# Optimization experiments

Measured on AMD Instinct MI355X. Metric: run time of the kernel, lower is better.

Reference implementation:

```python
import jax, jax.numpy as jnp
import numpy as np

N_NODES = 50000
N_EDGES = 800000
IN_CH = 128
OUT_CH = 32
HID = 2 * OUT_CH  # 64


def setup_inputs() -> dict:
    key = jax.random.key(0)
    ks = jax.random.split(key, 8)
    x = jax.random.normal(ks[0], (N_NODES, IN_CH), dtype=jnp.float32)
    edge_index = jax.random.randint(ks[1], (2, N_EDGES), 0, N_NODES, dtype=jnp.int32)
    s1 = 1.0 / np.sqrt(IN_CH)
    s2 = 1.0 / np.sqrt(HID)
    W1 = jax.random.normal(ks[2], (IN_CH, HID), dtype=jnp.float32) * s1
    b1 = jnp.zeros((HID,), dtype=jnp.float32)
    W_mu = jax.random.normal(ks[3], (HID, OUT_CH), dtype=jnp.float32) * s2
    b_mu = jnp.zeros((OUT_CH,), dtype=jnp.float32)
    W_logstd = jax.random.normal(ks[4], (HID, OUT_CH), dtype=jnp.float32) * s2
    b_logstd = jnp.zeros((OUT_CH,), dtype=jnp.float32)
    return {"x": x, "edge_index": edge_index, "W1": W1, "b1": b1,
            "W_mu": W_mu, "b_mu": b_mu, "W_logstd": W_logstd, "b_logstd": b_logstd}


def _gcn_norm(edge_index, n, dtype):
    # PyG GCNConv: add self-loops, symmetric normalization D^-1/2 A D^-1/2
    loops = jnp.arange(n, dtype=edge_index.dtype)
    src = jnp.concatenate([edge_index[0], loops])
    dst = jnp.concatenate([edge_index[1], loops])
    deg = jax.ops.segment_sum(jnp.ones_like(dst, dtype=dtype), dst, num_segments=n)
    deg_inv_sqrt = jnp.where(deg > 0, jax.lax.rsqrt(deg), 0.0)
    norm = deg_inv_sqrt[src] * deg_inv_sqrt[dst]  # [E+N]
    return src, dst, norm


def _gcn_conv(x, W, b, src, dst, norm, n):
    h = x @ W                        # transform first (in >= out)
    msg = h[src] * norm[:, None]     # gather + scale, [E+N, out]
    out = jax.ops.segment_sum(msg, dst, num_segments=n)
    return out + b


def reference(x, edge_index, W1, b1, W_mu, b_mu, W_logstd, b_logstd):
    n = x.shape[0]
    src, dst, norm = _gcn_norm(edge_index, n, x.dtype)
    h = jax.nn.relu(_gcn_conv(x, W1, b1, src, dst, norm, n))
    mu = _gcn_conv(h, W_mu, b_mu, src, dst, norm, n)
    logstd = _gcn_conv(h, W_logstd, b_logstd, src, dst, norm, n)
    return mu, logstd
```

## Files before the change

kernel.cpp:

```cpp
#include <hip/hip_runtime.h>
#include <hip/hip_fp16.h>

#define N_NODES 50000
#define N_EDGES 800000
#define IN_CH 128
#define HID 64
#define OUT_CH 32
#define CAP 64
#define ZROW N_NODES
#define PART_SZ 6250

union H4 { uint2 u; __half2 h[2]; };

__global__ __launch_bounds__(256) void k_scatter(const int* __restrict__ ei,
                                                 int* cur, unsigned short* __restrict__ pk,
                                                 unsigned* zA, unsigned* zB) {
    if (blockIdx.x == 0) {
        int t = threadIdx.x;
        if (t < 32) zA[t] = 0u;
        else if (t < 64) zB[t - 32] = 0u;
    }
    int part = blockIdx.x & 7;
    int g = (blockIdx.x >> 3) * 256 + threadIdx.x;
    if (g >= N_EDGES / 2) return;
    int2 dd = ((const int2*)(ei + N_EDGES))[g];
    bool a0 = (unsigned)(dd.x - part * PART_SZ) < (unsigned)PART_SZ;
    bool a1 = (unsigned)(dd.y - part * PART_SZ) < (unsigned)PART_SZ;
    if (!a0 && !a1) return;
    int2 ss = ((const int2*)ei)[g];
    if (a0) {
        int n = atomicAdd(&cur[dd.x], 1);
        int slot = (n < 32) ? (((n & 3) << 3) | (n >> 2)) : n;
        pk[(dd.x << 6) + slot] = (unsigned short)ss.x;
    }
    if (a1) {
        int n = atomicAdd(&cur[dd.y], 1);
        int slot = (n < 32) ? (((n & 3) << 3) | (n >> 2)) : n;
        pk[(dd.y << 6) + slot] = (unsigned short)ss.y;
    }
}

__global__ __launch_bounds__(256) void k_mm1(const float* __restrict__ x,
                                             const float* __restrict__ W1,
                                             const int* __restrict__ cur,
                                             __half* __restrict__ t1) {
    __shared__ float4 ws[64 * 16];
    __shared__ float  xsT[64 * 64];
    int t = threadIdx.x;
    int n0 = blockIdx.x * 64;
    int lane = t & 63, wv_ = t >> 6;
    int ni = lane >> 2;
    int cq = ((lane & 3) << 2) + wv_;
    const float4* W4 = (const float4*)W1;
    const float4* x4 = (const float4*)x;
    float4 acc0 = {0,0,0,0}, acc1 = acc0, acc2 = acc0, acc3 = acc0;
#pragma unroll
    for (int kt = 0; kt < 2; ++kt) {
        __syncthreads();
#pragma unroll
        for (int i = 0; i < 4; ++i) {
            int L = i * 256 + t;
            ws[L] = W4[kt * 1024 + L];
            int n = L >> 4, q = L & 15;
            int ng = n0 + n; if (ng >= N_NODES) ng = N_NODES - 1;
            float4 v = x4[ng * 32 + kt * 16 + q];
            int fb = q * 256 + (((n >> 2) ^ q) << 2) + (n & 3);
            xsT[fb]       = v.x;
            xsT[fb + 64]  = v.y;
            xsT[fb + 128] = v.z;
            xsT[fb + 192] = v.w;
        }
        __syncthreads();
        const float4* xsT4 = (const float4*)xsT;
#pragma unroll 8
        for (int k = 0; k < 64; ++k) {
            float4 xv = xsT4[k * 16 + (ni ^ (k >> 2))];
            float4 wvv = ws[k * 16 + cq];
            acc0.x += xv.x * wvv.x; acc0.y += xv.x * wvv.y; acc0.z += xv.x * wvv.z; acc0.w += xv.x * wvv.w;
            acc1.x += xv.y * wvv.x; acc1.y += xv.y * wvv.y; acc1.z += xv.y * wvv.z; acc1.w += xv.y * wvv.w;
            acc2.x += xv.z * wvv.x; acc2.y += xv.z * wvv.y; acc2.z += xv.z * wvv.z; acc2.w += xv.z * wvv.w;
            acc3.x += xv.w * wvv.x; acc3.y += xv.w * wvv.y; acc3.z += xv.w * wvv.z; acc3.w += xv.w * wvv.w;
        }
    }
    int nb = n0 + 4 * ni;
    if (nb < N_NODES) {
        int4 c4 = *(const int4*)(cur + nb);
        float d0 = rsqrtf((float)c4.x + 1.0f);
        float d1 = rsqrtf((float)c4.y + 1.0f);
        float d2 = rsqrtf((float)c4.z + 1.0f);
        float d3 = rsqrtf((float)c4.w + 1.0f);
        uint2* o2 = (uint2*)t1;
        H4 v;
        v.h[0] = __floats2half2_rn(d0 * acc0.x, d0 * acc0.y);
        v.h[1] = __floats2half2_rn(d0 * acc0.z, d0 * acc0.w);
        o2[(nb + 0) * 16 + cq] = v.u;
        v.h[0] = __floats2half2_rn(d1 * acc1.x, d1 * acc1.y);
        v.h[1] = __floats2half2_rn(d1 * acc1.z, d1 * acc1.w);
        o2[(nb + 1) * 16 + cq] = v.u;
        v.h[0] = __floats2half2_rn(d2 * acc2.x, d2 * acc2.y);
        v.h[1] = __floats2half2_rn(d2 * acc2.z, d2 * acc2.w);
        o2[(nb + 2) * 16 + cq] = v.u;
        v.h[0] = __floats2half2_rn(d3 * acc3.x, d3 * acc3.y);
        v.h[1] = __floats2half2_rn(d3 * acc3.z, d3 * acc3.w);
        o2[(nb + 3) * 16 + cq] = v.u;
    }
}

__global__ __launch_bounds__(256) void k_agg(const unsigned short* __restrict__ pk,
                                             const int* __restrict__ cur,
                                             const __half* __restrict__ in,
                                             const float* __restrict__ bias,
                                             __half* __restrict__ out,
                                             int apply_relu) {
    int wave = (blockIdx.x * 256 + threadIdx.x) >> 6;
    if (wave >= N_NODES / 2) return;
    int lane = threadIdx.x & 63;
    int half = lane >> 5;
    int eg = (lane >> 3) & 3;
    int cs = lane & 7;
    int w = wave * 2 + half;
    int cnt = cur[w];
    int rowb = w << 6;
    const uint4* __restrict__ inv = (const uint4*)in;

    uint4 pp = *(const uint4*)(pk + rowb + (eg << 3));
    const unsigned short* us = (const unsigned short*)&pp;
    int sidx[8];
#pragma unroll
    for (int j = 0; j < 8; ++j)
        sidx[j] = (eg + 4 * j < cnt) ? (int)us[j] : ZROW;
    int sself = (eg == 0) ? w : ZROW;
    uint4 r0 = inv[sidx[0] * 8 + cs];
    uint4 r1 = inv[sidx[1] * 8 + cs];
    uint4 r2 = inv[sidx[2] * 8 + cs];
    uint4 r3 = inv[sidx[3] * 8 + cs];
    uint4 r4 = inv[sidx[4] * 8 + cs];
    uint4 r5 = inv[sidx[5] * 8 + cs];
    uint4 r6 = inv[sidx[6] * 8 + cs];
    uint4 r7 = inv[sidx[7] * 8 + cs];
    uint4 rs = inv[sself * 8 + cs];
    float acc[8] = {0,0,0,0,0,0,0,0};
#define ACC8(R) { const __half2* h2 = (const __half2*)&(R); float2 f;          \
        f = __half22float2(h2[0]); acc[0] += f.x; acc[1] += f.y;               \
        f = __half22float2(h2[1]); acc[2] += f.x; acc[3] += f.y;               \
        f = __half22float2(h2[2]); acc[4] += f.x; acc[5] += f.y;               \
        f = __half22float2(h2[3]); acc[6] += f.x; acc[7] += f.y; }
    ACC8(r0); ACC8(r1); ACC8(r2); ACC8(r3);
    ACC8(r4); ACC8(r5); ACC8(r6); ACC8(r7);
    ACC8(rs);

    for (int n = 32 + eg; n < cnt; n += 4) {
        int s = (int)pk[rowb + n];
        uint4 r = inv[s * 8 + cs];
        ACC8(r);
    }
#undef ACC8
#pragma unroll
    for (int m = 8; m <= 16; m <<= 1)
#pragma unroll
        for (int i = 0; i < 8; ++i) acc[i] += __shfl_xor(acc[i], m, 64);
    if (eg == 0) {
        float dw = rsqrtf((float)cnt + 1.0f);
        if (apply_relu) {
            float4 b0 = ((const float4*)bias)[2 * cs];
            float4 b1v = ((const float4*)bias)[2 * cs + 1];
            acc[0] = dw * fmaxf(dw * acc[0] + b0.x, 0.f);
            acc[1] = dw * fmaxf(dw * acc[1] + b0.y, 0.f);
            acc[2] = dw * fmaxf(dw * acc[2] + b0.z, 0.f);
            acc[3] = dw * fmaxf(dw * acc[3] + b0.w, 0.f);
            acc[4] = dw * fmaxf(dw * acc[4] + b1v.x, 0.f);
            acc[5] = dw * fmaxf(dw * acc[5] + b1v.y, 0.f);
            acc[6] = dw * fmaxf(dw * acc[6] + b1v.z, 0.f);
            acc[7] = dw * fmaxf(dw * acc[7] + b1v.w, 0.f);
        } else {
#pragma unroll
            for (int i = 0; i < 8; ++i) acc[i] *= dw;
        }
        __half2 o[4];
        o[0] = __floats2half2_rn(acc[0], acc[1]);
        o[1] = __floats2half2_rn(acc[2], acc[3]);
        o[2] = __floats2half2_rn(acc[4], acc[5]);
        o[3] = __floats2half2_rn(acc[6], acc[7]);
        ((uint4*)out)[w * 8 + cs] = *(const uint4*)o;
    }
}

__global__ __launch_bounds__(256) void k_mm2(const __half* __restrict__ agg2,
                                             const float* __restrict__ Wmu,
                                             const float* __restrict__ bmu,
                                             const float* __restrict__ Wls,
                                             const float* __restrict__ bls,
                                             float* __restrict__ out) {
    __shared__ float4 ws[64 * 16];
    __shared__ float  xsT[64 * 64];
    int t = threadIdx.x;
    int n0 = blockIdx.x * 64;
    int lane = t & 63, wv_ = t >> 6;
    int ni = lane >> 2;
    int cq = ((lane & 3) << 2) + wv_;
    const float4* Wm4 = (const float4*)Wmu;
    const float4* Wl4 = (const float4*)Wls;
    const uint2*  x2  = (const uint2*)agg2;
#pragma unroll
    for (int i = 0; i < 4; ++i) {
        int L = i * 256 + t;
        int k = L >> 4, c = L & 15;
        ws[L] = (c < 8) ? Wm4[k * 8 + c] : Wl4[k * 8 + (c - 8)];
        int n = L >> 4, q = L & 15;
        int ng = n0 + n; if (ng >= N_NODES) ng = N_NODES - 1;
        H4 hv; hv.u = x2[ng * 16 + q];
        float2 f0 = __half22float2(hv.h[0]), f1 = __half22float2(hv.h[1]);
        int fb = q * 256 + (((n >> 2) ^ q) << 2) + (n & 3);
        xsT[fb]       = f0.x;
        xsT[fb + 64]  = f0.y;
        xsT[fb + 128] = f1.x;
        xsT[fb + 192] = f1.y;
    }
    float4 b = (cq < 8) ? ((const float4*)bmu)[cq] : ((const float4*)bls)[cq - 8];
    float4 acc0 = b, acc1 = b, acc2 = b, acc3 = b;
    __syncthreads();
    const float4* xsT4 = (const float4*)xsT;
#pragma unroll 8
    for (int k = 0; k < 64; ++k) {
        float4 xv = xsT4[k * 16 + (ni ^ (k >> 2))];
        float4 wvv = ws[k * 16 + cq];
        acc0.x += xv.x * wvv.x; acc0.y += xv.x * wvv.y; acc0.z += xv.x * wvv.z; acc0.w += xv.x * wvv.w;
        acc1.x += xv.y * wvv.x; acc1.y += xv.y * wvv.y; acc1.z += xv.y * wvv.z; acc1.w += xv.y * wvv.w;
        acc2.x += xv.z * wvv.x; acc2.y += xv.z * wvv.y; acc2.z += xv.z * wvv.z; acc2.w += xv.z * wvv.w;
        acc3.x += xv.w * wvv.x; acc3.y += xv.w * wvv.y; acc3.z += xv.w * wvv.z; acc3.w += xv.w * wvv.w;
    }
    int nb = n0 + 4 * ni;
    if (nb < N_NODES) {
        float4* o4 = (float4*)out;
        long base_off = (cq < 8) ? 0 : (long)N_NODES * 8;
        int cq8 = cq & 7;
        o4[base_off + (long)(nb + 0) * 8 + cq8] = acc0;
        o4[base_off + (long)(nb + 1) * 8 + cq8] = acc1;
        o4[base_off + (long)(nb + 2) * 8 + cq8] = acc2;
        o4[base_off + (long)(nb + 3) * 8 + cq8] = acc3;
    }
}

extern "C" void kernel_launch(void* const* d_in, const int* in_sizes, int n_in,
                              void* d_out, int out_size, void* d_ws, size_t ws_size,
                              hipStream_t stream) {
    const float* x   = (const float*)d_in[0];
    const int*   ei  = (const int*)  d_in[1];
    const float* W1  = (const float*)d_in[2];
    const float* b1  = (const float*)d_in[3];
    const float* Wmu = (const float*)d_in[4];
    const float* bmu = (const float*)d_in[5];
    const float* Wls = (const float*)d_in[6];
    const float* bls = (const float*)d_in[7];
    float* out = (float*)d_out;

    int*   cur  = (int*)d_ws;
    unsigned short* pk = (unsigned short*)((int*)d_ws + 50176);
    __half* bufA = (__half*)((int*)d_ws + 1650176);
    __half* bufB = (__half*)((int*)d_ws + 3250304);
    __half* bufC = (__half*)((int*)d_ws + 4850432);

    hipMemsetAsync(d_ws, 0, 200000, stream);
    k_scatter <<<1563 * 8, 256, 0, stream>>>(ei, cur, pk,
                   (unsigned*)(bufA + (size_t)ZROW * HID),
                   (unsigned*)(bufB + (size_t)ZROW * HID));
    k_mm1 <<<782, 256, 0, stream>>>(x, W1, cur, bufA);
    k_agg <<<6250, 256, 0, stream>>>(pk, cur, bufA, b1, bufB, 1);
    k_agg <<<6250, 256, 0, stream>>>(pk, cur, bufB, nullptr, bufC, 0);
    k_mm2 <<<782, 256, 0, stream>>>(bufC, Wmu, bmu, Wls, bls, out);
}
```

Baseline: 184.4 us.

## Replace 8-pass partitioned edge scatter with two-pass bucket-then-scatter CSR build

Edge insertion into per-destination adjacency lists used to run 8 partitioned passes, each rereading the whole edge list and keeping only destinations in its node range. Now one kernel reads every edge once and bins packed (dst,src) records into per-block segment buffers by destination partition, using shared-memory counters. A second kernel is ordered by bucket so that its atomics and pk writes stay local to one partition range. This removes 7 of the 8 rereads of edge_index at the cost of an extra kernel launch and a round trip of the packed records through memory.

Result: no change. 187.6 us (+1.8%).

```diff
diff --git a/kernel.cpp b/kernel.cpp
--- a/kernel.cpp
+++ b/kernel.cpp
@@ -9,35 +9,65 @@
 #define CAP 64
 #define ZROW N_NODES
 #define PART_SZ 6250
+#define NSEG 1563
+#define SEGCAP 128
 
 union H4 { uint2 u; __half2 h[2]; };
 
-__global__ __launch_bounds__(256) void k_scatter(const int* __restrict__ ei,
-                                                 int* cur, unsigned short* __restrict__ pk,
-                                                 unsigned* zA, unsigned* zB) {
+__global__ __launch_bounds__(256) void k_bucket(const int* __restrict__ ei,
+                                                int* cur, int* __restrict__ segcnt,
+                                                unsigned* __restrict__ segbuf,
+                                                unsigned short* __restrict__ pk,
+                                                unsigned* zA, unsigned* zB) {
+    __shared__ int lcnt[8];
+    int t = threadIdx.x;
     if (blockIdx.x == 0) {
-        int t = threadIdx.x;
         if (t < 32) zA[t] = 0u;
         else if (t < 64) zB[t - 32] = 0u;
     }
-    int part = blockIdx.x & 7;
-    int g = (blockIdx.x >> 3) * 256 + threadIdx.x;
-    if (g >= N_EDGES / 2) return;
-    int2 dd = ((const int2*)(ei + N_EDGES))[g];
-    bool a0 = (unsigned)(dd.x - part * PART_SZ) < (unsigned)PART_SZ;
-    bool a1 = (unsigned)(dd.y - part * PART_SZ) < (unsigned)PART_SZ;
-    if (!a0 && !a1) return;
-    int2 ss = ((const int2*)ei)[g];
-    if (a0) {
-        int n = atomicAdd(&cur[dd.x], 1);
-        int slot = (n < 32) ? (((n & 3) << 3) | (n >> 2)) : n;
-        pk[(dd.x << 6) + slot] = (unsigned short)ss.x;
-    }
-    if (a1) {
-        int n = atomicAdd(&cur[dd.y], 1);
-        int slot = (n < 32) ? (((n & 3) << 3) | (n >> 2)) : n;
-        pk[(dd.y << 6) + slot] = (unsigned short)ss.y;
-    }
+    if (t < 8) lcnt[t] = 0;
+    __syncthreads();
+    int g = blockIdx.x * 256 + t;
+    if (g < N_EDGES / 2) {
+        int2 ss = ((const int2*)ei)[g];
+        int2 dd = ((const int2*)(ei + N_EDGES))[g];
+        int b0 = dd.x / PART_SZ;
+        int b1 = dd.y / PART_SZ;
+        int s0 = atomicAdd(&lcnt[b0], 1);
+        int s1 = atomicAdd(&lcnt[b1], 1);
+        unsigned base = blockIdx.x * (8u * SEGCAP);
+        if (s0 < SEGCAP) segbuf[base + b0 * SEGCAP + s0] = ((unsigned)dd.x << 16) | (unsigned)ss.x;
+        else { int n = atomicAdd(&cur[dd.x], 1);
+               int sl = (n < 32) ? (((n & 3) << 3) | (n >> 2)) : n;
+               pk[(dd.x << 6) + sl] = (unsigned short)ss.x; }
+        if (s1 < SEGCAP) segbuf[base + b1 * SEGCAP + s1] = ((unsigned)dd.y << 16) | (unsigned)ss.y;
+        else { int n = atomicAdd(&cur[dd.y], 1);
+               int sl = (n < 32) ? (((n & 3) << 3) | (n >> 2)) : n;
+               pk[(dd.y << 6) + sl] = (unsigned short)ss.y; }
+    }
+    __syncthreads();
+    if (t < 8) segcnt[blockIdx.x * 8 + t] = lcnt[t];
+}
+
+__global__ __launch_bounds__(256) void k_scatter2(const int* __restrict__ segcnt,
+                                                  const unsigned* __restrict__ segbuf,
+                                                  int* cur,
+                                                  unsigned short* __restrict__ pk) {
+    int i = blockIdx.x;
+    int bucket = i & 7;
+    int p = i >> 3;
+    int t = threadIdx.x;
+    int seg = 2 * p + (t >> 7);
+    int slot = t & 127;
+    if (seg >= NSEG) return;
+    int c = segcnt[seg * 8 + bucket];
+    if (slot >= c) return;
+    unsigned rec = segbuf[seg * (8u * SEGCAP) + bucket * SEGCAP + slot];
+    int dst = (int)(rec >> 16);
+    int src = (int)(rec & 0xffffu);
+    int n = atomicAdd(&cur[dst], 1);
+    int sl = (n < 32) ? (((n & 3) << 3) | (n >> 2)) : n;
+    pk[(dst << 6) + sl] = (unsigned short)src;
 }
 
 __global__ __launch_bounds__(256) void k_mm1(const float* __restrict__ x,
@@ -254,16 +284,19 @@
     const float* bls = (const float*)d_in[7];
     float* out = (float*)d_out;
 
-    int*   cur  = (int*)d_ws;
-    unsigned short* pk = (unsigned short*)((int*)d_ws + 50176);
-    __half* bufA = (__half*)((int*)d_ws + 1650176);
-    __half* bufB = (__half*)((int*)d_ws + 3250304);
-    __half* bufC = (__half*)((int*)d_ws + 4850432);
+    int*      cur    = (int*)d_ws;
+    int*      segcnt = (int*)d_ws + 50048;
+    unsigned* segbuf = (unsigned*)d_ws + 62560;
+    unsigned short* pk = (unsigned short*)((int*)d_ws + 1663072);
+    __half* bufA = (__half*)((int*)d_ws + 3263072);
+    __half* bufB = (__half*)((int*)d_ws + 4863104);
+    __half* bufC = (__half*)((int*)d_ws + 6463136);
 
     hipMemsetAsync(d_ws, 0, 200000, stream);
-    k_scatter <<<1563 * 8, 256, 0, stream>>>(ei, cur, pk,
+    k_bucket   <<<NSEG, 256, 0, stream>>>(ei, cur, segcnt, segbuf, pk,
                    (unsigned*)(bufA + (size_t)ZROW * HID),
                    (unsigned*)(bufB + (size_t)ZROW * HID));
+    k_scatter2 <<<782 * 8, 256, 0, stream>>>(segcnt, segbuf, cur, pk);
     k_mm1 <<<782, 256, 0, stream>>>(x, W1, cur, bufA);
     k_agg <<<6250, 256, 0, stream>>>(pk, cur, bufA, b1, bufB, 1);
     k_agg <<<6250, 256, 0, stream>>>(pk, cur, bufB, nullptr, bufC, 0);
```
